# Kernel optimization log

Measured on AMD Instinct MI355X. Metric: run time of the kernel, lower is better.

The kernel has to match this reference:

```python
import jax, jax.numpy as jnp
import numpy as np

DT = 0.1
TAU = 1.0

def setup_inputs() -> dict:
    key = jax.random.key(0)
    ks = jax.random.split(key, 5)
    B, T, IN_C, N, R, OUT_C = 64, 1024, 16, 512, 16, 8
    return {
        "Batch_Input": jax.random.normal(ks[0], (B, T, IN_C), dtype=jnp.float32),
        "In_w": jax.random.normal(ks[1], (N, IN_C), dtype=jnp.float32),
        "V_w": jax.random.normal(ks[2], (R, N), dtype=jnp.float32) / np.float32(np.sqrt(N)),
        "U_w": jax.random.normal(ks[3], (N, R), dtype=jnp.float32) / np.float32(np.sqrt(R)),
        "Out_w": jax.random.normal(ks[4], (OUT_C, N), dtype=jnp.float32),
        "hidden_0": jnp.zeros((N,), dtype=jnp.float32),
    }

def reference(Batch_Input, In_w, V_w, U_w, Out_w, hidden_0):
    # Eval-mode forward (no noise injection), faithful to the torch math.
    B, T, _ = Batch_Input.shape
    a = DT / TAU  # leak integration coefficient
    # Input projection: [B, T, in_C] @ [in_C, N] -> [B, T, N]
    Inp = jnp.einsum('bti,ni->btn', Batch_Input, In_w)
    h0 = jnp.broadcast_to(hidden_0, (B, hidden_0.shape[0]))
    Inp_t = jnp.transpose(Inp, (1, 0, 2))  # [T, B, N] for scan

    def step(h, inp_t):
        phi = jnp.tanh(h)                       # act_func = Tanh
        low = jnp.einsum('bn,rn->br', phi, V_w)  # V: N -> r
        rec = jnp.einsum('br,nr->bn', low, U_w)  # U: r -> N
        h_new = (1.0 - a) * h + a * (rec + inp_t)
        return h_new, h_new

    _, hs = jax.lax.scan(step, h0, Inp_t)       # hs: [T, B, N]
    hidden_t = jnp.transpose(hs, (1, 0, 2))      # [B, T, N]
    out = jnp.einsum('btn,on->bto', jnp.tanh(hidden_t), Out_w)  # [B, T, out_C]
    return hidden_t, out
```

## Files before the change

kernel.cpp:

```cpp
#include <hip/hip_runtime.h>

#define BATCH 64
#define TT    1024
#define INC   16
#define NN    512
#define RNK   16
#define OUTC  8

#define A_COEF 0.1f

__device__ __forceinline__ float fast_tanh(float x) {
    float e = __expf(2.0f * x);
    return 1.0f - __fdividef(2.0f, e + 1.0f);
}

__device__ __forceinline__ void lgkm_barrier() {
    asm volatile("s_waitcnt lgkmcnt(0)\n\ts_barrier" ::: "memory");
}

template<int CTRL>
__device__ __forceinline__ float dpp_add(float x) {
    int y = __builtin_amdgcn_update_dpp(0, __float_as_int(x), CTRL, 0xF, 0xF, true);
    return x + __int_as_float(y);
}

__device__ __forceinline__ float half_wave_sum(float x) {
    x = dpp_add<0x111>(x);
    x = dpp_add<0x112>(x);
    x = dpp_add<0x114>(x);
    x = dpp_add<0x118>(x);
    x = dpp_add<0x142>(x);
    return x;
}

__device__ __forceinline__ float wave_sum(float x) {
    x = half_wave_sum(x);
    x = dpp_add<0x143>(x);
    return x;
}

__global__ __launch_bounds__(512, 1) void scan_kernel(
    const float* __restrict__ x,
    const float* __restrict__ In_w,
    const float* __restrict__ V_w,
    const float* __restrict__ U_w,
    const float* __restrict__ Out_w,
    const float* __restrict__ h0,
    float* __restrict__ hidden,
    float* __restrict__ out)
{
    const int b   = blockIdx.x;
    const int tid = threadIdx.x;
    const int rr  = tid >> 5;
    const int g   = tid & 31;
    const int ow  = tid >> 6;
    const int p   = tid & 63;

    __shared__ __align__(16) float xs[TT * INC];
    __shared__ __align__(16) float phi_s[NN];
    __shared__ __align__(16) float low_s[RNK];

    {
        const float4* src = (const float4*)(x + (size_t)b * TT * INC);
        float4* dst = (float4*)xs;
        #pragma unroll
        for (int c = 0; c < 8; ++c)
            dst[c * 512 + tid] = src[c * 512 + tid];
    }

    float Ur[RNK];
    #pragma unroll
    for (int r = 0; r < RNK; ++r) Ur[r] = U_w[tid * RNK + r];

    float Wr[INC];
    #pragma unroll
    for (int i = 0; i < INC; ++i) Wr[i] = In_w[tid * INC + i];

    float Vr[16];
    #pragma unroll
    for (int k = 0; k < 4; ++k)
        #pragma unroll
        for (int j = 0; j < 4; ++j)
            Vr[k * 4 + j] = V_w[rr * NN + k * 128 + g * 4 + j];

    float Owr[8];
    #pragma unroll
    for (int j = 0; j < 8; ++j) Owr[j] = Out_w[ow * NN + p * 8 + j];

    float h = h0[tid];

    __syncthreads();

    float* hb = hidden + (size_t)b * TT * NN;
    float* ob = out + (size_t)b * TT * OUTC;

    float4 xv0, xv1, xv2, xv3;
    {
        const float4* xp = (const float4*)xs;
        xv0 = xp[0]; xv1 = xp[1]; xv2 = xp[2]; xv3 = xp[3];
    }

    for (int t = 0; t < TT; ++t) {
        float phi = fast_tanh(h);
        phi_s[tid] = phi;

        float ia = Wr[0] * xv0.x;
        float ib = Wr[1] * xv0.y;
        float ic = Wr[2] * xv0.z;
        float id = Wr[3] * xv0.w;
        ia = fmaf(Wr[4],  xv1.x, ia);
        ib = fmaf(Wr[5],  xv1.y, ib);
        ic = fmaf(Wr[6],  xv1.z, ic);
        id = fmaf(Wr[7],  xv1.w, id);
        ia = fmaf(Wr[8],  xv2.x, ia);
        ib = fmaf(Wr[9],  xv2.y, ib);
        ic = fmaf(Wr[10], xv2.z, ic);
        id = fmaf(Wr[11], xv2.w, id);
        ia = fmaf(Wr[12], xv3.x, ia);
        ib = fmaf(Wr[13], xv3.y, ib);
        ic = fmaf(Wr[14], xv3.z, ic);
        id = fmaf(Wr[15], xv3.w, id);
        float inp = (ia + ib) + (ic + id);

        lgkm_barrier();

        float p0 = 0.f, p1 = 0.f, p2 = 0.f, p3 = 0.f;
        #pragma unroll
        for (int k = 0; k < 4; ++k) {
            float4 ph = *(const float4*)&phi_s[k * 128 + g * 4];
            p0 = fmaf(Vr[k * 4 + 0], ph.x, p0);
            p1 = fmaf(Vr[k * 4 + 1], ph.y, p1);
            p2 = fmaf(Vr[k * 4 + 2], ph.z, p2);
            p3 = fmaf(Vr[k * 4 + 3], ph.w, p3);
        }
        float partial = (p0 + p1) + (p2 + p3);
        partial = half_wave_sum(partial);
        if (g == 31) low_s[rr] = partial;

        {
            int tn = (t + 1 < TT) ? t + 1 : t;
            const float4* xp = (const float4*)(xs + tn * INC);
            xv0 = xp[0]; xv1 = xp[1]; xv2 = xp[2]; xv3 = xp[3];
        }

        float4 q0 = *(const float4*)&phi_s[p * 8];
        float4 q1 = *(const float4*)&phi_s[p * 8 + 4];
        float oa = Owr[0] * q0.x;
        float obb = Owr[1] * q0.y;
        float oc = Owr[2] * q0.z;
        float od = Owr[3] * q0.w;
        oa  = fmaf(Owr[4], q1.x, oa);
        obb = fmaf(Owr[5], q1.y, obb);
        oc  = fmaf(Owr[6], q1.z, oc);
        od  = fmaf(Owr[7], q1.w, od);
        float osum = (oa + obb) + (oc + od);
        osum = wave_sum(osum);
        if (t > 0 && p == 63)
            ob[(t - 1) * OUTC + ow] = osum;

        lgkm_barrier();

        float4 l0 = *(const float4*)&low_s[0];
        float4 l1 = *(const float4*)&low_s[4];
        float4 l2 = *(const float4*)&low_s[8];
        float4 l3 = *(const float4*)&low_s[12];
        float ra = Ur[0] * l0.x;
        float rb = Ur[1] * l0.y;
        float rc = Ur[2] * l0.z;
        float rd = Ur[3] * l0.w;
        ra = fmaf(Ur[4],  l1.x, ra);
        rb = fmaf(Ur[5],  l1.y, rb);
        rc = fmaf(Ur[6],  l1.z, rc);
        rd = fmaf(Ur[7],  l1.w, rd);
        ra = fmaf(Ur[8],  l2.x, ra);
        rb = fmaf(Ur[9],  l2.y, rb);
        rc = fmaf(Ur[10], l2.z, rc);
        rd = fmaf(Ur[11], l2.w, rd);
        ra = fmaf(Ur[12], l3.x, ra);
        rb = fmaf(Ur[13], l3.y, rb);
        rc = fmaf(Ur[14], l3.z, rc);
        rd = fmaf(Ur[15], l3.w, rd);
        float rec = (ra + rb) + (rc + rd);

        h = fmaf(A_COEF, (rec + inp) - h, h);
        hb[t * NN + tid] = h;
    }

    float phi = fast_tanh(h);
    phi_s[tid] = phi;
    lgkm_barrier();
    {
        float4 q0 = *(const float4*)&phi_s[p * 8];
        float4 q1 = *(const float4*)&phi_s[p * 8 + 4];
        float oa = Owr[0] * q0.x;
        float obb = Owr[1] * q0.y;
        float oc = Owr[2] * q0.z;
        float od = Owr[3] * q0.w;
        oa  = fmaf(Owr[4], q1.x, oa);
        obb = fmaf(Owr[5], q1.y, obb);
        oc  = fmaf(Owr[6], q1.z, oc);
        od  = fmaf(Owr[7], q1.w, od);
        float osum = (oa + obb) + (oc + od);
        osum = wave_sum(osum);
        if (p == 63)
            ob[(TT - 1) * OUTC + ow] = osum;
    }
}

extern "C" void kernel_launch(void* const* d_in, const int* in_sizes, int n_in,
                              void* d_out, int out_size, void* d_ws, size_t ws_size,
                              hipStream_t stream) {
    const float* x    = (const float*)d_in[0];
    const float* In_w = (const float*)d_in[1];
    const float* V_w  = (const float*)d_in[2];
    const float* U_w  = (const float*)d_in[3];
    const float* Ow   = (const float*)d_in[4];
    const float* h0   = (const float*)d_in[5];

    float* hidden = (float*)d_out;
    float* out    = hidden + (size_t)BATCH * TT * NN;

    scan_kernel<<<BATCH, 512, 0, stream>>>(x, In_w, V_w, U_w, Ow, h0, hidden, out);
}
```

Measured before the change: 810.5 us.

## Split input projection and output readout out of the sequential scan kernel

Result: slower. 879.3 us (+8.5%).

```diff
diff --git a/kernel.cpp b/kernel.cpp
--- a/kernel.cpp
+++ b/kernel.cpp
@@ -6,6 +6,7 @@
 #define NN    512
 #define RNK   16
 #define OUTC  8
+#define BT    (BATCH * TT)
 
 #define A_COEF 0.1f
 
@@ -24,139 +25,129 @@
     return x + __int_as_float(y);
 }
 
-__device__ __forceinline__ float half_wave_sum(float x) {
+__device__ __forceinline__ float wave_sum(float x) {
     x = dpp_add<0x111>(x);
     x = dpp_add<0x112>(x);
     x = dpp_add<0x114>(x);
     x = dpp_add<0x118>(x);
     x = dpp_add<0x142>(x);
-    return x;
-}
-
-__device__ __forceinline__ float wave_sum(float x) {
-    x = half_wave_sum(x);
     x = dpp_add<0x143>(x);
     return x;
 }
 
-__global__ __launch_bounds__(512, 1) void scan_kernel(
+__global__ __launch_bounds__(512) void inp_kernel(
     const float* __restrict__ x,
     const float* __restrict__ In_w,
+    float* __restrict__ Inp)
+{
+    const int n = threadIdx.x;
+    const int row0 = blockIdx.x * 32;
+
+    float W[INC];
+    #pragma unroll
+    for (int k = 0; k < 4; ++k) {
+        float4 w = *(const float4*)&In_w[n * INC + k * 4];
+        W[k*4+0] = w.x; W[k*4+1] = w.y; W[k*4+2] = w.z; W[k*4+3] = w.w;
+    }
+
+    #pragma unroll 4
+    for (int r = 0; r < 32; ++r) {
+        const int row = row0 + r;
+        const float4* xr = (const float4*)(x + (size_t)row * INC);
+        float4 a = xr[0], bq = xr[1], c = xr[2], d = xr[3];
+        float s0 = W[0]  * a.x;
+        float s1 = W[1]  * a.y;
+        float s2 = W[2]  * a.z;
+        float s3 = W[3]  * a.w;
+        s0 = fmaf(W[4],  bq.x, s0);
+        s1 = fmaf(W[5],  bq.y, s1);
+        s2 = fmaf(W[6],  bq.z, s2);
+        s3 = fmaf(W[7],  bq.w, s3);
+        s0 = fmaf(W[8],  c.x, s0);
+        s1 = fmaf(W[9],  c.y, s1);
+        s2 = fmaf(W[10], c.z, s2);
+        s3 = fmaf(W[11], c.w, s3);
+        s0 = fmaf(W[12], d.x, s0);
+        s1 = fmaf(W[13], d.y, s1);
+        s2 = fmaf(W[14], d.z, s2);
+        s3 = fmaf(W[15], d.w, s3);
+        Inp[(size_t)row * NN + n] = (s0 + s1) + (s2 + s3);
+    }
+}
+
+__global__ __launch_bounds__(512, 1) void scan_kernel(
+    const float* __restrict__ Inp,
     const float* __restrict__ V_w,
     const float* __restrict__ U_w,
-    const float* __restrict__ Out_w,
     const float* __restrict__ h0,
-    float* __restrict__ hidden,
-    float* __restrict__ out)
+    float* __restrict__ hidden)
 {
     const int b   = blockIdx.x;
     const int tid = threadIdx.x;
-    const int rr  = tid >> 5;
-    const int g   = tid & 31;
-    const int ow  = tid >> 6;
+    const int w   = tid >> 6;
     const int p   = tid & 63;
 
-    __shared__ __align__(16) float xs[TT * INC];
     __shared__ __align__(16) float phi_s[NN];
     __shared__ __align__(16) float low_s[RNK];
 
-    {
-        const float4* src = (const float4*)(x + (size_t)b * TT * INC);
-        float4* dst = (float4*)xs;
-        #pragma unroll
-        for (int c = 0; c < 8; ++c)
-            dst[c * 512 + tid] = src[c * 512 + tid];
-    }
-
     float Ur[RNK];
     #pragma unroll
-    for (int r = 0; r < RNK; ++r) Ur[r] = U_w[tid * RNK + r];
-
-    float Wr[INC];
-    #pragma unroll
-    for (int i = 0; i < INC; ++i) Wr[i] = In_w[tid * INC + i];
-
-    float Vr[16];
-    #pragma unroll
-    for (int k = 0; k < 4; ++k)
-        #pragma unroll
-        for (int j = 0; j < 4; ++j)
-            Vr[k * 4 + j] = V_w[rr * NN + k * 128 + g * 4 + j];
-
-    float Owr[8];
-    #pragma unroll
-    for (int j = 0; j < 8; ++j) Owr[j] = Out_w[ow * NN + p * 8 + j];
+    for (int k = 0; k < 4; ++k) {
+        float4 u = *(const float4*)&U_w[tid * RNK + k * 4];
+        Ur[k*4+0] = u.x; Ur[k*4+1] = u.y; Ur[k*4+2] = u.z; Ur[k*4+3] = u.w;
+    }
+
+    float Va[8], Vb[8];
+    #pragma unroll
+    for (int j = 0; j < 2; ++j) {
+        float4 va = *(const float4*)&V_w[(2*w)   * NN + j * 256 + 4 * p];
+        float4 vb = *(const float4*)&V_w[(2*w+1) * NN + j * 256 + 4 * p];
+        Va[j*4+0] = va.x; Va[j*4+1] = va.y; Va[j*4+2] = va.z; Va[j*4+3] = va.w;
+        Vb[j*4+0] = vb.x; Vb[j*4+1] = vb.y; Vb[j*4+2] = vb.z; Vb[j*4+3] = vb.w;
+    }
 
     float h = h0[tid];
 
+    const float* ib = Inp + (size_t)b * TT * NN + tid;
+    float* hb = hidden + (size_t)b * TT * NN + tid;
+
+    float inp_c = ib[0];
+    float inp_n = ib[NN];
+
     __syncthreads();
-
-    float* hb = hidden + (size_t)b * TT * NN;
-    float* ob = out + (size_t)b * TT * OUTC;
-
-    float4 xv0, xv1, xv2, xv3;
-    {
-        const float4* xp = (const float4*)xs;
-        xv0 = xp[0]; xv1 = xp[1]; xv2 = xp[2]; xv3 = xp[3];
-    }
 
     for (int t = 0; t < TT; ++t) {
         float phi = fast_tanh(h);
         phi_s[tid] = phi;
 
-        float ia = Wr[0] * xv0.x;
-        float ib = Wr[1] * xv0.y;
-        float ic = Wr[2] * xv0.z;
-        float id = Wr[3] * xv0.w;
-        ia = fmaf(Wr[4],  xv1.x, ia);
-        ib = fmaf(Wr[5],  xv1.y, ib);
-        ic = fmaf(Wr[6],  xv1.z, ic);
-        id = fmaf(Wr[7],  xv1.w, id);
-        ia = fmaf(Wr[8],  xv2.x, ia);
-        ib = fmaf(Wr[9],  xv2.y, ib);
-        ic = fmaf(Wr[10], xv2.z, ic);
-        id = fmaf(Wr[11], xv2.w, id);
-        ia = fmaf(Wr[12], xv3.x, ia);
-        ib = fmaf(Wr[13], xv3.y, ib);
-        ic = fmaf(Wr[14], xv3.z, ic);
-        id = fmaf(Wr[15], xv3.w, id);
-        float inp = (ia + ib) + (ic + id);
-
         lgkm_barrier();
 
-        float p0 = 0.f, p1 = 0.f, p2 = 0.f, p3 = 0.f;
-        #pragma unroll
-        for (int k = 0; k < 4; ++k) {
-            float4 ph = *(const float4*)&phi_s[k * 128 + g * 4];
-            p0 = fmaf(Vr[k * 4 + 0], ph.x, p0);
-            p1 = fmaf(Vr[k * 4 + 1], ph.y, p1);
-            p2 = fmaf(Vr[k * 4 + 2], ph.z, p2);
-            p3 = fmaf(Vr[k * 4 + 3], ph.w, p3);
-        }
-        float partial = (p0 + p1) + (p2 + p3);
-        partial = half_wave_sum(partial);
-        if (g == 31) low_s[rr] = partial;
-
-        {
-            int tn = (t + 1 < TT) ? t + 1 : t;
-            const float4* xp = (const float4*)(xs + tn * INC);
-            xv0 = xp[0]; xv1 = xp[1]; xv2 = xp[2]; xv3 = xp[3];
-        }
-
-        float4 q0 = *(const float4*)&phi_s[p * 8];
-        float4 q1 = *(const float4*)&phi_s[p * 8 + 4];
-        float oa = Owr[0] * q0.x;
-        float obb = Owr[1] * q0.y;
-        float oc = Owr[2] * q0.z;
-        float od = Owr[3] * q0.w;
-        oa  = fmaf(Owr[4], q1.x, oa);
-        obb = fmaf(Owr[5], q1.y, obb);
-        oc  = fmaf(Owr[6], q1.z, oc);
-        od  = fmaf(Owr[7], q1.w, od);
-        float osum = (oa + obb) + (oc + od);
-        osum = wave_sum(osum);
-        if (t > 0 && p == 63)
-            ob[(t - 1) * OUTC + ow] = osum;
+        float4 ph0 = *(const float4*)&phi_s[4 * p];
+        float4 ph1 = *(const float4*)&phi_s[256 + 4 * p];
+
+        float pa0 = Va[0] * ph0.x;
+        float pa1 = Va[1] * ph0.y;
+        float pb0 = Vb[0] * ph0.x;
+        float pb1 = Vb[1] * ph0.y;
+        pa0 = fmaf(Va[2], ph0.z, pa0);
+        pa1 = fmaf(Va[3], ph0.w, pa1);
+        pb0 = fmaf(Vb[2], ph0.z, pb0);
+        pb1 = fmaf(Vb[3], ph0.w, pb1);
+        pa0 = fmaf(Va[4], ph1.x, pa0);
+        pa1 = fmaf(Va[5], ph1.y, pa1);
+        pb0 = fmaf(Vb[4], ph1.x, pb0);
+        pb1 = fmaf(Vb[5], ph1.y, pb1);
+        pa0 = fmaf(Va[6], ph1.z, pa0);
+        pa1 = fmaf(Va[7], ph1.w, pa1);
+        pb0 = fmaf(Vb[6], ph1.z, pb0);
+        pb1 = fmaf(Vb[7], ph1.w, pb1);
+        float pa = wave_sum(pa0 + pa1);
+        float pb = wave_sum(pb0 + pb1);
+        if (p == 63)
+            *(float2*)&low_s[2 * w] = make_float2(pa, pb);
+
+        int tn = (t + 2 < TT) ? t + 2 : TT - 1;
+        float inp_f = ib[(size_t)tn * NN];
 
         lgkm_barrier();
 
@@ -182,28 +173,58 @@
         rd = fmaf(Ur[15], l3.w, rd);
         float rec = (ra + rb) + (rc + rd);
 
-        h = fmaf(A_COEF, (rec + inp) - h, h);
-        hb[t * NN + tid] = h;
-    }
-
-    float phi = fast_tanh(h);
-    phi_s[tid] = phi;
-    lgkm_barrier();
-    {
-        float4 q0 = *(const float4*)&phi_s[p * 8];
-        float4 q1 = *(const float4*)&phi_s[p * 8 + 4];
-        float oa = Owr[0] * q0.x;
-        float obb = Owr[1] * q0.y;
-        float oc = Owr[2] * q0.z;
-        float od = Owr[3] * q0.w;
-        oa  = fmaf(Owr[4], q1.x, oa);
-        obb = fmaf(Owr[5], q1.y, obb);
-        oc  = fmaf(Owr[6], q1.z, oc);
-        od  = fmaf(Owr[7], q1.w, od);
-        float osum = (oa + obb) + (oc + od);
-        osum = wave_sum(osum);
-        if (p == 63)
-            ob[(TT - 1) * OUTC + ow] = osum;
+        h = fmaf(A_COEF, (rec + inp_c) - h, h);
+        hb[(size_t)t * NN] = h;
+
+        inp_c = inp_n;
+        inp_n = inp_f;
+    }
+}
+
+__global__ __launch_bounds__(256) void out_kernel(
+    const float* __restrict__ hidden,
+    const float* __restrict__ Out_w,
+    float* __restrict__ out)
+{
+    const int lane = threadIdx.x & 63;
+    const int wv   = threadIdx.x >> 6;
+    const int gw   = blockIdx.x * 4 + wv;
+
+    float Ow[OUTC][8];
+    #pragma unroll
+    for (int o = 0; o < OUTC; ++o) {
+        float4 w0 = *(const float4*)&Out_w[o * NN + lane * 8];
+        float4 w1 = *(const float4*)&Out_w[o * NN + lane * 8 + 4];
+        Ow[o][0] = w0.x; Ow[o][1] = w0.y; Ow[o][2] = w0.z; Ow[o][3] = w0.w;
+        Ow[o][4] = w1.x; Ow[o][5] = w1.y; Ow[o][6] = w1.z; Ow[o][7] = w1.w;
+    }
+
+    #pragma unroll 2
+    for (int rr = 0; rr < 32; ++rr) {
+        const int row = gw * 32 + rr;
+        const float* hr = hidden + (size_t)row * NN + lane * 8;
+        float4 a0 = *(const float4*)&hr[0];
+        float4 a1 = *(const float4*)&hr[4];
+        float ph[8];
+        ph[0] = fast_tanh(a0.x); ph[1] = fast_tanh(a0.y);
+        ph[2] = fast_tanh(a0.z); ph[3] = fast_tanh(a0.w);
+        ph[4] = fast_tanh(a1.x); ph[5] = fast_tanh(a1.y);
+        ph[6] = fast_tanh(a1.z); ph[7] = fast_tanh(a1.w);
+
+        float acc[OUTC];
+        #pragma unroll
+        for (int o = 0; o < OUTC; ++o) {
+            float s = Ow[o][0] * ph[0];
+            #pragma unroll
+            for (int j = 1; j < 8; ++j) s = fmaf(Ow[o][j], ph[j], s);
+            acc[o] = wave_sum(s);
+        }
+        if (lane == 63) {
+            float4 r0 = make_float4(acc[0], acc[1], acc[2], acc[3]);
+            float4 r1 = make_float4(acc[4], acc[5], acc[6], acc[7]);
+            *(float4*)&out[(size_t)row * OUTC]     = r0;
+            *(float4*)&out[(size_t)row * OUTC + 4] = r1;
+        }
     }
 }
 
@@ -219,6 +240,9 @@
 
     float* hidden = (float*)d_out;
     float* out    = hidden + (size_t)BATCH * TT * NN;
-
-    scan_kernel<<<BATCH, 512, 0, stream>>>(x, In_w, V_w, U_w, Ow, h0, hidden, out);
-}
+    float* Inp    = (float*)d_ws;
+
+    inp_kernel<<<BT / 32, 512, 0, stream>>>(x, In_w, Inp);
+    scan_kernel<<<BATCH, 512, 0, stream>>>(Inp, V_w, U_w, h0, hidden);
+    out_kernel<<<512, 256, 0, stream>>>(hidden, Ow, out);
+}
```

## Halve block size so each thread owns two neurons with quad-DPP broadcast of low

Applied to the files above, without the earlier changes.

New measurement: 871.7 us. 7.5% more time.

```diff
diff --git a/kernel.cpp b/kernel.cpp
--- a/kernel.cpp
+++ b/kernel.cpp
@@ -24,22 +24,24 @@
     return x + __int_as_float(y);
 }
 
-__device__ __forceinline__ float half_wave_sum(float x) {
+__device__ __forceinline__ float wave_sum(float x) {
     x = dpp_add<0x111>(x);
     x = dpp_add<0x112>(x);
     x = dpp_add<0x114>(x);
     x = dpp_add<0x118>(x);
     x = dpp_add<0x142>(x);
-    return x;
-}
-
-__device__ __forceinline__ float wave_sum(float x) {
-    x = half_wave_sum(x);
     x = dpp_add<0x143>(x);
     return x;
 }
 
-__global__ __launch_bounds__(512, 1) void scan_kernel(
+template<int K>
+__device__ __forceinline__ float quad_bcast(float x) {
+    constexpr int ctrl = K * 0x55;
+    int y = __builtin_amdgcn_update_dpp(0, __float_as_int(x), ctrl, 0xF, 0xF, true);
+    return __int_as_float(y);
+}
+
+__global__ __launch_bounds__(256, 1) void scan_kernel(
     const float* __restrict__ x,
     const float* __restrict__ In_w,
     const float* __restrict__ V_w,
@@ -51,10 +53,9 @@
 {
     const int b   = blockIdx.x;
     const int tid = threadIdx.x;
-    const int rr  = tid >> 5;
-    const int g   = tid & 31;
-    const int ow  = tid >> 6;
+    const int w   = tid >> 6;
     const int p   = tid & 63;
+    const int q   = p & 3;
 
     __shared__ __align__(16) float xs[TT * INC];
     __shared__ __align__(16) float phi_s[NN];
@@ -64,146 +65,203 @@
         const float4* src = (const float4*)(x + (size_t)b * TT * INC);
         float4* dst = (float4*)xs;
         #pragma unroll
-        for (int c = 0; c < 8; ++c)
-            dst[c * 512 + tid] = src[c * 512 + tid];
-    }
-
-    float Ur[RNK];
+        for (int c = 0; c < 16; ++c)
+            dst[c * 256 + tid] = src[c * 256 + tid];
+    }
+
+    float U0[RNK], U1[RNK];
     #pragma unroll
-    for (int r = 0; r < RNK; ++r) Ur[r] = U_w[tid * RNK + r];
-
-    float Wr[INC];
+    for (int k = 0; k < 4; ++k) {
+        float4 u = *(const float4*)&U_w[tid * RNK + k * 4];
+        U0[k*4+0] = u.x; U0[k*4+1] = u.y; U0[k*4+2] = u.z; U0[k*4+3] = u.w;
+        float4 v = *(const float4*)&U_w[(tid + 256) * RNK + k * 4];
+        U1[k*4+0] = v.x; U1[k*4+1] = v.y; U1[k*4+2] = v.z; U1[k*4+3] = v.w;
+    }
+    float W0[INC], W1[INC];
     #pragma unroll
-    for (int i = 0; i < INC; ++i) Wr[i] = In_w[tid * INC + i];
-
-    float Vr[16];
+    for (int k = 0; k < 4; ++k) {
+        float4 a = *(const float4*)&In_w[tid * INC + k * 4];
+        W0[k*4+0] = a.x; W0[k*4+1] = a.y; W0[k*4+2] = a.z; W0[k*4+3] = a.w;
+        float4 c = *(const float4*)&In_w[(tid + 256) * INC + k * 4];
+        W1[k*4+0] = c.x; W1[k*4+1] = c.y; W1[k*4+2] = c.z; W1[k*4+3] = c.w;
+    }
+    float V[4][8];
     #pragma unroll
-    for (int k = 0; k < 4; ++k)
-        #pragma unroll
-        for (int j = 0; j < 4; ++j)
-            Vr[k * 4 + j] = V_w[rr * NN + k * 128 + g * 4 + j];
-
-    float Owr[8];
-    #pragma unroll
-    for (int j = 0; j < 8; ++j) Owr[j] = Out_w[ow * NN + p * 8 + j];
-
-    float h = h0[tid];
+    for (int rr = 0; rr < 4; ++rr) {
+        const int r = 4 * w + rr;
+        float4 va = *(const float4*)&V_w[r * NN + 4 * p];
+        float4 vb = *(const float4*)&V_w[r * NN + 256 + 4 * p];
+        V[rr][0] = va.x; V[rr][1] = va.y; V[rr][2] = va.z; V[rr][3] = va.w;
+        V[rr][4] = vb.x; V[rr][5] = vb.y; V[rr][6] = vb.z; V[rr][7] = vb.w;
+    }
+    float O0[8], O1[8];
+    {
+        float4 a = *(const float4*)&Out_w[(2*w) * NN + 4 * p];
+        float4 c = *(const float4*)&Out_w[(2*w) * NN + 256 + 4 * p];
+        O0[0]=a.x; O0[1]=a.y; O0[2]=a.z; O0[3]=a.w;
+        O0[4]=c.x; O0[5]=c.y; O0[6]=c.z; O0[7]=c.w;
+        float4 d = *(const float4*)&Out_w[(2*w+1) * NN + 4 * p];
+        float4 e = *(const float4*)&Out_w[(2*w+1) * NN + 256 + 4 * p];
+        O1[0]=d.x; O1[1]=d.y; O1[2]=d.z; O1[3]=d.w;
+        O1[4]=e.x; O1[5]=e.y; O1[6]=e.z; O1[7]=e.w;
+    }
+
+    float h0v = h0[tid];
+    float h1v = h0[tid + 256];
 
     __syncthreads();
 
     float* hb = hidden + (size_t)b * TT * NN;
     float* ob = out + (size_t)b * TT * OUTC;
 
-    float4 xv0, xv1, xv2, xv3;
+    float4 xc0, xc1, xc2, xc3;
     {
         const float4* xp = (const float4*)xs;
-        xv0 = xp[0]; xv1 = xp[1]; xv2 = xp[2]; xv3 = xp[3];
+        xc0 = xp[0]; xc1 = xp[1]; xc2 = xp[2]; xc3 = xp[3];
     }
 
     for (int t = 0; t < TT; ++t) {
-        float phi = fast_tanh(h);
-        phi_s[tid] = phi;
-
-        float ia = Wr[0] * xv0.x;
-        float ib = Wr[1] * xv0.y;
-        float ic = Wr[2] * xv0.z;
-        float id = Wr[3] * xv0.w;
-        ia = fmaf(Wr[4],  xv1.x, ia);
-        ib = fmaf(Wr[5],  xv1.y, ib);
-        ic = fmaf(Wr[6],  xv1.z, ic);
-        id = fmaf(Wr[7],  xv1.w, id);
-        ia = fmaf(Wr[8],  xv2.x, ia);
-        ib = fmaf(Wr[9],  xv2.y, ib);
-        ic = fmaf(Wr[10], xv2.z, ic);
-        id = fmaf(Wr[11], xv2.w, id);
-        ia = fmaf(Wr[12], xv3.x, ia);
-        ib = fmaf(Wr[13], xv3.y, ib);
-        ic = fmaf(Wr[14], xv3.z, ic);
-        id = fmaf(Wr[15], xv3.w, id);
-        float inp = (ia + ib) + (ic + id);
+        float phi0 = fast_tanh(h0v);
+        float phi1 = fast_tanh(h1v);
+        phi_s[tid]       = phi0;
+        phi_s[tid + 256] = phi1;
+
+        float i0a = W0[0]  * xc0.x,  i0b = W0[1]  * xc0.y;
+        float i0c = W0[2]  * xc0.z,  i0d = W0[3]  * xc0.w;
+        float i1a = W1[0]  * xc0.x,  i1b = W1[1]  * xc0.y;
+        float i1c = W1[2]  * xc0.z,  i1d = W1[3]  * xc0.w;
+        i0a = fmaf(W0[4],  xc1.x, i0a);  i0b = fmaf(W0[5],  xc1.y, i0b);
+        i0c = fmaf(W0[6],  xc1.z, i0c);  i0d = fmaf(W0[7],  xc1.w, i0d);
+        i1a = fmaf(W1[4],  xc1.x, i1a);  i1b = fmaf(W1[5],  xc1.y, i1b);
+        i1c = fmaf(W1[6],  xc1.z, i1c);  i1d = fmaf(W1[7],  xc1.w, i1d);
+        i0a = fmaf(W0[8],  xc2.x, i0a);  i0b = fmaf(W0[9],  xc2.y, i0b);
+        i0c = fmaf(W0[10], xc2.z, i0c);  i0d = fmaf(W0[11], xc2.w, i0d);
+        i1a = fmaf(W1[8],  xc2.x, i1a);  i1b = fmaf(W1[9],  xc2.y, i1b);
+        i1c = fmaf(W1[10], xc2.z, i1c);  i1d = fmaf(W1[11], xc2.w, i1d);
+        i0a = fmaf(W0[12], xc3.x, i0a);  i0b = fmaf(W0[13], xc3.y, i0b);
+        i0c = fmaf(W0[14], xc3.z, i0c);  i0d = fmaf(W0[15], xc3.w, i0d);
+        i1a = fmaf(W1[12], xc3.x, i1a);  i1b = fmaf(W1[13], xc3.y, i1b);
+        i1c = fmaf(W1[14], xc3.z, i1c);  i1d = fmaf(W1[15], xc3.w, i1d);
+        float inp0 = (i0a + i0b) + (i0c + i0d);
+        float inp1 = (i1a + i1b) + (i1c + i1d);
 
         lgkm_barrier();
 
-        float p0 = 0.f, p1 = 0.f, p2 = 0.f, p3 = 0.f;
+        float4 ph0 = *(const float4*)&phi_s[4 * p];
+        float4 ph1 = *(const float4*)&phi_s[256 + 4 * p];
+
+        float pr[4];
         #pragma unroll
-        for (int k = 0; k < 4; ++k) {
-            float4 ph = *(const float4*)&phi_s[k * 128 + g * 4];
-            p0 = fmaf(Vr[k * 4 + 0], ph.x, p0);
-            p1 = fmaf(Vr[k * 4 + 1], ph.y, p1);
-            p2 = fmaf(Vr[k * 4 + 2], ph.z, p2);
-            p3 = fmaf(Vr[k * 4 + 3], ph.w, p3);
+        for (int rr = 0; rr < 4; ++rr) {
+            float a = V[rr][0] * ph0.x;
+            float bq = V[rr][1] * ph0.y;
+            a  = fmaf(V[rr][2], ph0.z, a);
+            bq = fmaf(V[rr][3], ph0.w, bq);
+            a  = fmaf(V[rr][4], ph1.x, a);
+            bq = fmaf(V[rr][5], ph1.y, bq);
+            a  = fmaf(V[rr][6], ph1.z, a);
+            bq = fmaf(V[rr][7], ph1.w, bq);
+            pr[rr] = a + bq;
         }
-        float partial = (p0 + p1) + (p2 + p3);
-        partial = half_wave_sum(partial);
-        if (g == 31) low_s[rr] = partial;
+        pr[0] = wave_sum(pr[0]);
+        pr[1] = wave_sum(pr[1]);
+        pr[2] = wave_sum(pr[2]);
+        pr[3] = wave_sum(pr[3]);
+        if (p == 63)
+            *(float4*)&low_s[4 * w] = make_float4(pr[0], pr[1], pr[2], pr[3]);
+
+        float oa = O0[0] * ph0.x;
+        float obq = O0[1] * ph0.y;
+        oa  = fmaf(O0[2], ph0.z, oa);
+        obq = fmaf(O0[3], ph0.w, obq);
+        oa  = fmaf(O0[4], ph1.x, oa);
+        obq = fmaf(O0[5], ph1.y, obq);
+        oa  = fmaf(O0[6], ph1.z, oa);
+        obq = fmaf(O0[7], ph1.w, obq);
+        float os0 = wave_sum(oa + obq);
+        float ca = O1[0] * ph0.x;
+        float cb = O1[1] * ph0.y;
+        ca = fmaf(O1[2], ph0.z, ca);
+        cb = fmaf(O1[3], ph0.w, cb);
+        ca = fmaf(O1[4], ph1.x, ca);
+        cb = fmaf(O1[5], ph1.y, cb);
+        ca = fmaf(O1[6], ph1.z, ca);
+        cb = fmaf(O1[7], ph1.w, cb);
+        float os1 = wave_sum(ca + cb);
+        if (t > 0 && p == 63)
+            *(float2*)&ob[(t - 1) * OUTC + 2 * w] = make_float2(os0, os1);
 
         {
             int tn = (t + 1 < TT) ? t + 1 : t;
             const float4* xp = (const float4*)(xs + tn * INC);
-            xv0 = xp[0]; xv1 = xp[1]; xv2 = xp[2]; xv3 = xp[3];
+            xc0 = xp[0]; xc1 = xp[1]; xc2 = xp[2]; xc3 = xp[3];
         }
 
-        float4 q0 = *(const float4*)&phi_s[p * 8];
-        float4 q1 = *(const float4*)&phi_s[p * 8 + 4];
-        float oa = Owr[0] * q0.x;
-        float obb = Owr[1] * q0.y;
-        float oc = Owr[2] * q0.z;
-        float od = Owr[3] * q0.w;
-        oa  = fmaf(Owr[4], q1.x, oa);
-        obb = fmaf(Owr[5], q1.y, obb);
-        oc  = fmaf(Owr[6], q1.z, oc);
-        od  = fmaf(Owr[7], q1.w, od);
-        float osum = (oa + obb) + (oc + od);
-        osum = wave_sum(osum);
-        if (t > 0 && p == 63)
-            ob[(t - 1) * OUTC + ow] = osum;
-
         lgkm_barrier();
 
-        float4 l0 = *(const float4*)&low_s[0];
-        float4 l1 = *(const float4*)&low_s[4];
-        float4 l2 = *(const float4*)&low_s[8];
-        float4 l3 = *(const float4*)&low_s[12];
-        float ra = Ur[0] * l0.x;
-        float rb = Ur[1] * l0.y;
-        float rc = Ur[2] * l0.z;
-        float rd = Ur[3] * l0.w;
-        ra = fmaf(Ur[4],  l1.x, ra);
-        rb = fmaf(Ur[5],  l1.y, rb);
-        rc = fmaf(Ur[6],  l1.z, rc);
-        rd = fmaf(Ur[7],  l1.w, rd);
-        ra = fmaf(Ur[8],  l2.x, ra);
-        rb = fmaf(Ur[9],  l2.y, rb);
-        rc = fmaf(Ur[10], l2.z, rc);
-        rd = fmaf(Ur[11], l2.w, rd);
-        ra = fmaf(Ur[12], l3.x, ra);
-        rb = fmaf(Ur[13], l3.y, rb);
-        rc = fmaf(Ur[14], l3.z, rc);
-        rd = fmaf(Ur[15], l3.w, rd);
-        float rec = (ra + rb) + (rc + rd);
-
-        h = fmaf(A_COEF, (rec + inp) - h, h);
-        hb[t * NN + tid] = h;
-    }
-
-    float phi = fast_tanh(h);
-    phi_s[tid] = phi;
+        float4 L = *(const float4*)&low_s[4 * q];
+        float Lg[16];
+        Lg[0]  = quad_bcast<0>(L.x);  Lg[1]  = quad_bcast<0>(L.y);
+        Lg[2]  = quad_bcast<0>(L.z);  Lg[3]  = quad_bcast<0>(L.w);
+        Lg[4]  = quad_bcast<1>(L.x);  Lg[5]  = quad_bcast<1>(L.y);
+        Lg[6]  = quad_bcast<1>(L.z);  Lg[7]  = quad_bcast<1>(L.w);
+        Lg[8]  = quad_bcast<2>(L.x);  Lg[9]  = quad_bcast<2>(L.y);
+        Lg[10] = quad_bcast<2>(L.z);  Lg[11] = quad_bcast<2>(L.w);
+        Lg[12] = quad_bcast<3>(L.x);  Lg[13] = quad_bcast<3>(L.y);
+        Lg[14] = quad_bcast<3>(L.z);  Lg[15] = quad_bcast<3>(L.w);
+
+        float r0a = U0[0] * Lg[0],  r0b = U0[1] * Lg[1];
+        float r0c = U0[2] * Lg[2],  r0d = U0[3] * Lg[3];
+        float r1a = U1[0] * Lg[0],  r1b = U1[1] * Lg[1];
+        float r1c = U1[2] * Lg[2],  r1d = U1[3] * Lg[3];
+        #pragma unroll
+        for (int k = 1; k < 4; ++k) {
+            r0a = fmaf(U0[4*k+0], Lg[4*k+0], r0a);
+            r0b = fmaf(U0[4*k+1], Lg[4*k+1], r0b);
+            r0c = fmaf(U0[4*k+2], Lg[4*k+2], r0c);
+            r0d = fmaf(U0[4*k+3], Lg[4*k+3], r0d);
+            r1a = fmaf(U1[4*k+0], Lg[4*k+0], r1a);
+            r1b = fmaf(U1[4*k+1], Lg[4*k+1], r1b);
+            r1c = fmaf(U1[4*k+2], Lg[4*k+2], r1c);
+            r1d = fmaf(U1[4*k+3], Lg[4*k+3], r1d);
+        }
+        float rec0 = (r0a + r0b) + (r0c + r0d);
+        float rec1 = (r1a + r1b) + (r1c + r1d);
+
+        h0v = fmaf(A_COEF, (rec0 + inp0) - h0v, h0v);
+        h1v = fmaf(A_COEF, (rec1 + inp1) - h1v, h1v);
+        hb[t * NN + tid]       = h0v;
+        hb[t * NN + tid + 256] = h1v;
+    }
+
+    float phi0 = fast_tanh(h0v);
+    float phi1 = fast_tanh(h1v);
+    phi_s[tid]       = phi0;
+    phi_s[tid + 256] = phi1;
     lgkm_barrier();
     {
-        float4 q0 = *(const float4*)&phi_s[p * 8];
-        float4 q1 = *(const float4*)&phi_s[p * 8 + 4];
-        float oa = Owr[0] * q0.x;
-        float obb = Owr[1] * q0.y;
-        float oc = Owr[2] * q0.z;
-        float od = Owr[3] * q0.w;
-        oa  = fmaf(Owr[4], q1.x, oa);
-        obb = fmaf(Owr[5], q1.y, obb);
-        oc  = fmaf(Owr[6], q1.z, oc);
-        od  = fmaf(Owr[7], q1.w, od);
-        float osum = (oa + obb) + (oc + od);
-        osum = wave_sum(osum);
+        float4 ph0 = *(const float4*)&phi_s[4 * p];
+        float4 ph1 = *(const float4*)&phi_s[256 + 4 * p];
+        float oa = O0[0] * ph0.x;
+        float obq = O0[1] * ph0.y;
+        oa  = fmaf(O0[2], ph0.z, oa);
+        obq = fmaf(O0[3], ph0.w, obq);
+        oa  = fmaf(O0[4], ph1.x, oa);
+        obq = fmaf(O0[5], ph1.y, obq);
+        oa  = fmaf(O0[6], ph1.z, oa);
+        obq = fmaf(O0[7], ph1.w, obq);
+        float os0 = wave_sum(oa + obq);
+        float ca = O1[0] * ph0.x;
+        float cb = O1[1] * ph0.y;
+        ca = fmaf(O1[2], ph0.z, ca);
+        cb = fmaf(O1[3], ph0.w, cb);
+        ca = fmaf(O1[4], ph1.x, ca);
+        cb = fmaf(O1[5], ph1.y, cb);
+        ca = fmaf(O1[6], ph1.z, ca);
+        cb = fmaf(O1[7], ph1.w, cb);
+        float os1 = wave_sum(ca + cb);
         if (p == 63)
-            ob[(TT - 1) * OUTC + ow] = osum;
+            *(float2*)&ob[(TT - 1) * OUTC + 2 * w] = make_float2(os0, os1);
     }
 }
 
@@ -220,5 +278,5 @@
     float* hidden = (float*)d_out;
     float* out    = hidden + (size_t)BATCH * TT * NN;
 
-    scan_kernel<<<BATCH, 512, 0, stream>>>(x, In_w, V_w, U_w, Ow, h0, hidden, out);
-}
+    scan_kernel<<<BATCH, 256, 0, stream>>>(x, In_w, V_w, U_w, Ow, h0, hidden, out);
+}
```
